# Kernel tuning notes

Hardware: AMD Instinct MI355X
Metric: run time of the kernel (lower is better)

## Reference

```python
import jax, jax.numpy as jnp
import numpy as np

N_QUBITS = 6
BLOCKS = 3
LATENT = 3
DIM = 1 << N_QUBITS  # 64, state-vector size
BATCH = 131072
INP_DIM = 6  # must equal N_QUBITS (repo applies linear_pre to the n_qubits-dim recon)

# Wire 0 is the most-significant qubit (PennyLane convention).
_idx = np.arange(DIM)
BITS = ((_idx[:, None] >> (N_QUBITS - 1 - np.arange(N_QUBITS))) & 1)  # (64, 6)
# Chain of CZ(k, k+1): all diagonal, fold into one sign vector per block.
CZ_SIGN = jnp.asarray(np.prod(1 - 2 * (BITS[:, :-1] * BITS[:, 1:]), axis=1).astype(np.float32))  # (64,)
Z_SIGNS = jnp.asarray((1 - 2 * BITS).astype(np.float32))  # (64, 6): <Z_k> signs per basis state


def _apply_1q(state, U, wire):
    # state: (B, 64) complex64; U: (2,2) complex64 acting on `wire`
    B = state.shape[0]
    s = state.reshape(B, 1 << wire, 2, 1 << (N_QUBITS - 1 - wire))
    s = jnp.einsum('ij,bxjy->bxiy', U, s)
    return s.reshape(B, DIM)


def _circuit(amps, weights, n_out):
    # AmplitudeEmbedding with normalize=True (x was already unit-normed in torch; idempotent)
    norm = jnp.linalg.norm(amps, axis=1, keepdims=True)
    state = (amps / norm).astype(jnp.complex64)  # (B, 64)
    for j in range(BLOCKS):
        for k in range(N_QUBITS):
            tx = weights[j, k, 0]
            tz = weights[j, k, 1]
            c = jnp.cos(0.5 * tx).astype(jnp.complex64)
            s = jnp.sin(0.5 * tx).astype(jnp.complex64)
            em = jnp.exp(-0.5j * tz).astype(jnp.complex64)
            ep = jnp.exp(0.5j * tz).astype(jnp.complex64)
            # Fused U = RZ(tz) @ RX(tx)
            U = jnp.stack([jnp.stack([em * c, -1j * em * s]),
                           jnp.stack([-1j * ep * s, ep * c])])
            state = _apply_1q(state, U, k)
        state = state * CZ_SIGN  # all CZ gates of the block, fused
    probs = state.real ** 2 + state.imag ** 2  # (B, 64)
    return probs @ Z_SIGNS[:, :n_out]  # expval(PauliZ(k)) for k < n_out


def setup_inputs() -> dict:
    key = jax.random.key(0)
    k1, k2, k3, k4, k5 = jax.random.split(key, 5)
    x = jax.random.normal(k1, (BATCH, INP_DIM), dtype=jnp.float32)
    bound = 1.0 / np.sqrt(INP_DIM)
    W_pre = jax.random.uniform(k2, (DIM, INP_DIM), minval=-bound, maxval=bound, dtype=jnp.float32)
    b_pre = jax.random.uniform(k3, (DIM,), minval=-bound, maxval=bound, dtype=jnp.float32)
    enc_w = jax.random.normal(k4, (BLOCKS, N_QUBITS, 3), dtype=jnp.float32) * 0.01
    dec_w = jax.random.normal(k5, (BLOCKS, N_QUBITS, 3), dtype=jnp.float32) * 0.01
    return {'x': x, 'W_pre': W_pre, 'b_pre': b_pre, 'enc_w': enc_w, 'dec_w': dec_w}


def reference(x, W_pre, b_pre, enc_w, dec_w):
    h = jnp.tanh(x @ W_pre.T + b_pre)                     # (B, 64)
    latent = _circuit(h, enc_w, LATENT)                    # (B, 3)
    padded = jnp.zeros((x.shape[0], DIM), jnp.float32).at[:, :LATENT].set(latent)
    recon = _circuit(padded, dec_w, N_QUBITS)              # (B, 6)
    reconstructed = jnp.tanh(recon @ W_pre.T + b_pre)      # (B, 64)
    return reconstructed, latent
```

## Files before the change

kernel.cpp:

```cpp
#include <hip/hip_runtime.h>

#define BATCH 131072

typedef float v2f __attribute__((ext_vector_type(2)));

__device__ __forceinline__ float fast_tanh(float v) {
    float e = __expf(2.0f * v);
    return 1.0f - 2.0f / (e + 1.0f);
}

template <int CTRL>
__device__ __forceinline__ float dppf(float v) {
    return __int_as_float(__builtin_amdgcn_update_dpp(
        0, __float_as_int(v), CTRL, 0xF, 0xF, true));
}
#define DPP_XOR1 0xB1
#define DPP_XOR2 0x4E

__device__ __forceinline__ v2f swap2(v2f v) { return __builtin_shufflevector(v, v, 1, 0); }

template <int MASK>
__device__ __forceinline__ void rx_pairs(v2f* zr, v2f* zi, float c, float s) {
#pragma unroll
    for (int j = 0; j < 8; ++j) {
        if (j & MASK) continue;
        int j1 = j | MASK;
        v2f ar = zr[j], ai = zi[j], br = zr[j1], bi = zi[j1];
        zr[j]  = c * ar + s * bi;
        zi[j]  = c * ai - s * br;
        zr[j1] = c * br + s * ai;
        zi[j1] = c * bi - s * ar;
    }
}

template <int CTRL>
__device__ __forceinline__ void rx_exch2(v2f* zr, v2f* zi, float c, float s) {
#pragma unroll
    for (int j = 0; j < 8; ++j) {
        v2f pr, pi;
        pr.x = dppf<CTRL>(zr[j].x);
        pr.y = dppf<CTRL>(zr[j].y);
        pi.x = dppf<CTRL>(zi[j].x);
        pi.y = dppf<CTRL>(zi[j].y);
        v2f mr = zr[j], mi = zi[j];
        zr[j] = c * mr + s * pi;
        zi[j] = c * mi - s * pr;
    }
}

__device__ __forceinline__ void enc_tail(v2f* zr, v2f* zi, const float* rx,
                                         const float* sDblk, int sub) {
    rx_pairs<2>(zr, zi, rx[2], rx[3]);
    rx_pairs<1>(zr, zi, rx[4], rx[5]);
    {
        float c = rx[6], s = rx[7];
#pragma unroll
        for (int j = 0; j < 8; ++j) {
            v2f orr = zr[j], oi = zi[j];
            zr[j] = c * orr + s * swap2(oi);
            zi[j] = c * oi - s * swap2(orr);
        }
    }
    rx_exch2<DPP_XOR2>(zr, zi, rx[8], rx[9]);
    rx_exch2<DPP_XOR1>(zr, zi, rx[10], rx[11]);
#pragma unroll
    for (int j = 0; j < 8; ++j) {
        float4 d = *(const float4*)&sDblk[(j * 4 + sub) * 4];
        v2f dr = {d.x, d.y}, di = {d.z, d.w};
        v2f orr = zr[j], oi = zi[j];
        zr[j] = dr * orr - di * oi;
        zi[j] = dr * oi + di * orr;
    }
}

__global__ __launch_bounds__(256, 4) void qae_fused(const float* __restrict__ x,
                                                    const float* __restrict__ Wp,
                                                    const float* __restrict__ bp,
                                                    const float* __restrict__ enc_w,
                                                    const float* __restrict__ dec_w,
                                                    float* __restrict__ out) {
    __shared__ __align__(16) float shbuf[1344];
    __shared__ float sA[36];
    __shared__ float sRx[36];

    float* gt = shbuf;
    float* Sr = shbuf + 144;
    float* Si = shbuf + 656;
    float* sW = shbuf;
    float* sB = shbuf + 544;
    float* sD = shbuf + 1088;

    const int t = threadIdx.x;
    const int bl = t >> 2;
    const int sub = t & 3;

    const size_t b = (size_t)blockIdx.x * 64 + bl;
    const float* xp = x + b * 6;
    float2 x01 = *(const float2*)(xp);
    float2 x23 = *(const float2*)(xp + 2);
    float2 x45 = *(const float2*)(xp + 4);

    if (t < 18) {
        float tx = dec_w[t * 3 + 0];
        float tz = dec_w[t * 3 + 1];
        float c = cosf(0.5f * tx), s = sinf(0.5f * tx);
        float ch = cosf(0.5f * tz), sh = sinf(0.5f * tz);
        gt[t * 8 + 0] = c * ch;  gt[t * 8 + 1] = -c * sh;
        gt[t * 8 + 2] = -s * sh; gt[t * 8 + 3] = -s * ch;
        gt[t * 8 + 4] = s * sh;  gt[t * 8 + 5] = -s * ch;
        gt[t * 8 + 6] = c * ch;  gt[t * 8 + 7] = c * sh;
        float etx = enc_w[t * 3 + 0];
        float ec = cosf(0.5f * etx), es = sinf(0.5f * etx);
        if (t >= 12) {
            sRx[2 * t] = ec * ec - es * es;
            sRx[2 * t + 1] = 4.0f * ec * es;
        } else {
            sRx[2 * t] = ec;
            sRx[2 * t + 1] = es;
        }
    }
    const int cl = t & 7;
    const int pr = t >> 3;
    for (int f = t; f < 512; f += 256) {
        int r = f >> 3, c = f & 7;
        Sr[f] = (r == c && c < 3) ? 1.0f : 0.0f;
        Si[f] = 0.0f;
    }

    for (int bb = 0; bb < 3; ++bb) {
        for (int w = 0; w < 6; ++w) {
            __syncthreads();
            int g = bb * 6 + w;
            int p = 5 - w;
            float u00r = gt[g * 8 + 0], u00i = gt[g * 8 + 1], u01r = gt[g * 8 + 2], u01i = gt[g * 8 + 3];
            float u10r = gt[g * 8 + 4], u10i = gt[g * 8 + 5], u11r = gt[g * 8 + 6], u11i = gt[g * 8 + 7];
            int r0 = ((pr >> p) << (p + 1)) | (pr & ((1 << p) - 1));
            int r1 = r0 | (1 << p);
            float ar = Sr[r0 * 8 + cl], ai = Si[r0 * 8 + cl];
            float br = Sr[r1 * 8 + cl], bi = Si[r1 * 8 + cl];
            Sr[r0 * 8 + cl] = u00r * ar - u00i * ai + u01r * br - u01i * bi;
            Si[r0 * 8 + cl] = u00r * ai + u00i * ar + u01r * bi + u01i * br;
            Sr[r1 * 8 + cl] = u10r * ar - u10i * ai + u11r * br - u11i * bi;
            Si[r1 * 8 + cl] = u10r * ai + u10i * ar + u11r * bi + u11i * br;
        }
        __syncthreads();
        for (int f = t; f < 512; f += 256) {
            int r = f >> 3;
            if (__popc(r & (r >> 1)) & 1) {
                Sr[f] = -Sr[f];
                Si[f] = -Si[f];
            }
        }
    }
    __syncthreads();

    if (t < 36) {
        int k = t / 6, i = t % 6;
        int d = (i < 3) ? i : ((i == 5) ? 1 : 0);
        int e = (i < 3) ? i : ((i == 3) ? 1 : 2);
        float acc = 0.0f;
        for (int r = 0; r < 64; ++r) {
            float term = Sr[r * 8 + d] * Sr[r * 8 + e] + Si[r * 8 + d] * Si[r * 8 + e];
            acc += ((r >> (5 - k)) & 1) ? -term : term;
        }
        if (i >= 3) acc *= 2.0f;
        sA[t] = acc;
    }
    __syncthreads();

    for (int f = t; f < 512; f += 256) {
        int g = f >> 4, e = f & 15;
        int j = g >> 2, su = g & 3;
        float val;
        if (e < 12)      { int row = 8 * j + su + 4 * (e & 1); val = Wp[row * 6 + (e >> 1)]; }
        else if (e < 14) { int row = 8 * j + su + 4 * (e - 12); val = bp[row]; }
        else val = 0.0f;
        sW[g * 16 + j * 4 + e] = val;
    }
    if (t < 64) {
        float w0 = Wp[t * 6 + 0], w1 = Wp[t * 6 + 1], w2 = Wp[t * 6 + 2];
        float w3 = Wp[t * 6 + 3], w4 = Wp[t * 6 + 4], w5 = Wp[t * 6 + 5];
        int basep = 8 * t + ((t >> 4) << 2);
#pragma unroll
        for (int i = 0; i < 6; ++i) {
            float acc = w0 * sA[0 * 6 + i] + w1 * sA[1 * 6 + i] + w2 * sA[2 * 6 + i]
                      + w3 * sA[3 * 6 + i] + w4 * sA[4 * 6 + i] + w5 * sA[5 * 6 + i];
            sB[basep + i] = acc;
        }
        sB[basep + 6] = bp[t];
        sB[basep + 7] = 0.0f;
    }
    if (t >= 64 && t < 192) {
        int idx = t - 64;
        int bb = idx >> 6, r = idx & 63;
        float phi = 0.0f;
        for (int k = 0; k < 6; ++k) {
            float tz = enc_w[(bb * 6 + k) * 3 + 1];
            phi += ((r >> (5 - k)) & 1) ? 0.5f * tz : -0.5f * tz;
        }
        float sgn = (__popc(r & (r >> 1)) & 1) ? -1.0f : 1.0f;
        int su = r & 3, m = r >> 2, j = m >> 1, hm = m & 1;
        int base = ((bb * 8 + j) * 4 + su) * 4;
        sD[base + hm]     = sgn * cosf(phi);
        sD[base + 2 + hm] = sgn * sinf(phi);
    }
    __syncthreads();

    float xv[6] = {x01.x, x01.y, x23.x, x23.y, x45.x, x45.y};

    v2f zr[8], zi[8];
    v2f S2 = {0.0f, 0.0f};
#pragma unroll
    for (int j = 0; j < 8; ++j) {
        const float* wb = &sW[(j * 4 + sub) * 16 + j * 4];
        float4 c0 = *(const float4*)wb;
        float4 c1 = *(const float4*)(wb + 4);
        float4 c2 = *(const float4*)(wb + 8);
        float4 c3 = *(const float4*)(wb + 12);
        v2f a = {c3.x, c3.y};
        a += xv[0] * (v2f){c0.x, c0.y};
        a += xv[1] * (v2f){c0.z, c0.w};
        a += xv[2] * (v2f){c1.x, c1.y};
        a += xv[3] * (v2f){c1.z, c1.w};
        a += xv[4] * (v2f){c2.x, c2.y};
        a += xv[5] * (v2f){c2.z, c2.w};
        v2f th = {fast_tanh(a.x), fast_tanh(a.y)};
        zr[j] = th;
        S2 += th * th;
    }
    float S = S2.x + S2.y;
    S += dppf<DPP_XOR1>(S);
    S += dppf<DPP_XOR2>(S);
    float invS = __builtin_amdgcn_rcpf(S);

    {
        const float* rx = sRx;
        float c = rx[0], s = rx[1];
#pragma unroll
        for (int j = 0; j < 4; ++j) {
            v2f a = zr[j], b2 = zr[j + 4];
            zr[j]     = c * a;
            zi[j]     = -s * b2;
            zr[j + 4] = c * b2;
            zi[j + 4] = -s * a;
        }
        enc_tail(zr, zi, rx, sD, sub);
    }
    {
        const float* rx = sRx + 12;
        rx_pairs<4>(zr, zi, rx[0], rx[1]);
        enc_tail(zr, zi, rx, sD + 128, sub);
    }

    v2f L0 = {0, 0}, L1 = {0, 0}, L2 = {0, 0};
#pragma unroll
    for (int j = 0; j < 8; ++j) {
        v2f p = zr[j] * zr[j] + zi[j] * zi[j];
        L0 += (j & 4) ? -p : p;
        L1 += (j & 2) ? -p : p;
        L2 += (j & 1) ? -p : p;
    }
    v2f Y0 = {0, 0}, Y1 = {0, 0}, Y2 = {0, 0};
#pragma unroll
    for (int j = 0; j < 4; ++j)
        Y0 += zr[j] * zi[j | 4] - zi[j] * zr[j | 4];
#pragma unroll
    for (int j0 = 0; j0 < 8; j0 += 4)
#pragma unroll
        for (int j = j0; j < j0 + 2; ++j)
            Y1 += zr[j] * zi[j | 2] - zi[j] * zr[j | 2];
#pragma unroll
    for (int j = 0; j < 8; j += 2)
        Y2 += zr[j] * zi[j | 1] - zi[j] * zr[j | 1];

    const float* p2 = sRx + 24;
    float t0 = p2[0] * (L0.x + L0.y) + p2[1] * (Y0.x + Y0.y);
    float t1 = p2[2] * (L1.x + L1.y) + p2[3] * (Y1.x + Y1.y);
    float t2 = p2[4] * (L2.x + L2.y) + p2[5] * (Y2.x + Y2.y);
    t0 += dppf<DPP_XOR1>(t0); t0 += dppf<DPP_XOR2>(t0);
    t1 += dppf<DPP_XOR1>(t1); t1 += dppf<DPP_XOR2>(t1);
    t2 += dppf<DPP_XOR1>(t2); t2 += dppf<DPP_XOR2>(t2);
    float l0 = t0 * invS, l1 = t1 * invS, l2 = t2 * invS;

    if (sub == 0) {
        size_t lo = (size_t)BATCH * 64 + b * 3;
        out[lo]     = l0;
        out[lo + 1] = l1;
        out[lo + 2] = l2;
    }

    float q0 = l0 * l0, q1 = l1 * l1, q2 = l2 * l2;
    float invr2 = __builtin_amdgcn_rcpf(q0 + q1 + q2);
    float qh0 = q0 * invr2, qh1 = q1 * invr2, qh2 = q2 * invr2;
    float qh3 = (l0 * l1) * invr2, qh4 = (l0 * l2) * invr2, qh5 = (l1 * l2) * invr2;

    const float* bB = &sB[132 * sub];
    const size_t ob = b * 64 + 16 * sub;
#pragma unroll
    for (int ch = 0; ch < 4; ++ch) {
        float v4[4];
#pragma unroll
        for (int r = 0; r < 4; ++r) {
            int qq = ch * 4 + r;
            float4 u0 = *(const float4*)&bB[8 * qq];
            float4 u1 = *(const float4*)&bB[8 * qq + 4];
            float acc = u1.z
                      + qh0 * u0.x + qh1 * u0.y + qh2 * u0.z + qh3 * u0.w
                      + qh4 * u1.x + qh5 * u1.y;
            v4[r] = fast_tanh(acc);
        }
        float4 o = {v4[0], v4[1], v4[2], v4[3]};
        *(float4*)&out[ob + ch * 4] = o;
    }
}

extern "C" void kernel_launch(void* const* d_in, const int* in_sizes, int n_in,
                              void* d_out, int out_size, void* d_ws, size_t ws_size,
                              hipStream_t stream) {
    const float* x   = (const float*)d_in[0];
    const float* Wp  = (const float*)d_in[1];
    const float* bpv = (const float*)d_in[2];
    const float* enc = (const float*)d_in[3];
    const float* dec = (const float*)d_in[4];
    float* out = (float*)d_out;

    qae_fused<<<(BATCH * 4) / 256, 256, 0, stream>>>(x, Wp, bpv, enc, dec, out);
}
```

Before: 102.6 us.

## Process two batch tiles per block and shrink decoder-unitary setup to four columns

Each block now handles two 64-sample tiles in a loop, so the per-block setup is amortized over twice the samples and only half as many blocks launch. That setup covers building the decoder unitary through 18 synchronized gate steps, the observable matrix, and the shared weight tables. The unitary scratch is also narrowed from 8 to 4 columns, so one element per thread suffices and only 128 threads do the gate updates. The cost is half as many blocks, and so less parallelism and latency hiding across the GPU. Each thread also holds x values for both tiles in registers.

```diff
diff --git a/kernel.cpp b/kernel.cpp
--- a/kernel.cpp
+++ b/kernel.cpp
@@ -1,6 +1,7 @@
 #include <hip/hip_runtime.h>
 
 #define BATCH 131072
+#define ITERS 2
 
 typedef float v2f __attribute__((ext_vector_type(2)));
 
@@ -85,7 +86,7 @@
 
     float* gt = shbuf;
     float* Sr = shbuf + 144;
-    float* Si = shbuf + 656;
+    float* Si = shbuf + 400;
     float* sW = shbuf;
     float* sB = shbuf + 544;
     float* sD = shbuf + 1088;
@@ -94,11 +95,15 @@
     const int bl = t >> 2;
     const int sub = t & 3;
 
-    const size_t b = (size_t)blockIdx.x * 64 + bl;
-    const float* xp = x + b * 6;
-    float2 x01 = *(const float2*)(xp);
-    float2 x23 = *(const float2*)(xp + 2);
-    float2 x45 = *(const float2*)(xp + 4);
+    const size_t b0 = (size_t)blockIdx.x * (64 * ITERS) + bl;
+    float2 xg[ITERS][3];
+#pragma unroll
+    for (int it = 0; it < ITERS; ++it) {
+        const float* xp = x + (b0 + (size_t)it * 64) * 6;
+        xg[it][0] = *(const float2*)(xp);
+        xg[it][1] = *(const float2*)(xp + 2);
+        xg[it][2] = *(const float2*)(xp + 4);
+    }
 
     if (t < 18) {
         float tx = dec_w[t * 3 + 0];
@@ -119,36 +124,38 @@
             sRx[2 * t + 1] = es;
         }
     }
-    const int cl = t & 7;
-    const int pr = t >> 3;
-    for (int f = t; f < 512; f += 256) {
-        int r = f >> 3, c = f & 7;
-        Sr[f] = (r == c && c < 3) ? 1.0f : 0.0f;
-        Si[f] = 0.0f;
-    }
-
+    {
+        int r = t >> 2, c = t & 3;
+        Sr[t] = (r == c && c < 3) ? 1.0f : 0.0f;
+        Si[t] = 0.0f;
+    }
+
+    const int cl = t & 3;
+    const int pr = t >> 2;
     for (int bb = 0; bb < 3; ++bb) {
         for (int w = 0; w < 6; ++w) {
             __syncthreads();
-            int g = bb * 6 + w;
-            int p = 5 - w;
-            float u00r = gt[g * 8 + 0], u00i = gt[g * 8 + 1], u01r = gt[g * 8 + 2], u01i = gt[g * 8 + 3];
-            float u10r = gt[g * 8 + 4], u10i = gt[g * 8 + 5], u11r = gt[g * 8 + 6], u11i = gt[g * 8 + 7];
-            int r0 = ((pr >> p) << (p + 1)) | (pr & ((1 << p) - 1));
-            int r1 = r0 | (1 << p);
-            float ar = Sr[r0 * 8 + cl], ai = Si[r0 * 8 + cl];
-            float br = Sr[r1 * 8 + cl], bi = Si[r1 * 8 + cl];
-            Sr[r0 * 8 + cl] = u00r * ar - u00i * ai + u01r * br - u01i * bi;
-            Si[r0 * 8 + cl] = u00r * ai + u00i * ar + u01r * bi + u01i * br;
-            Sr[r1 * 8 + cl] = u10r * ar - u10i * ai + u11r * br - u11i * bi;
-            Si[r1 * 8 + cl] = u10r * ai + u10i * ar + u11r * bi + u11i * br;
+            if (t < 128) {
+                int g = bb * 6 + w;
+                int p = 5 - w;
+                float u00r = gt[g * 8 + 0], u00i = gt[g * 8 + 1], u01r = gt[g * 8 + 2], u01i = gt[g * 8 + 3];
+                float u10r = gt[g * 8 + 4], u10i = gt[g * 8 + 5], u11r = gt[g * 8 + 6], u11i = gt[g * 8 + 7];
+                int r0 = ((pr >> p) << (p + 1)) | (pr & ((1 << p) - 1));
+                int r1 = r0 | (1 << p);
+                float ar = Sr[r0 * 4 + cl], ai = Si[r0 * 4 + cl];
+                float br = Sr[r1 * 4 + cl], bi = Si[r1 * 4 + cl];
+                Sr[r0 * 4 + cl] = u00r * ar - u00i * ai + u01r * br - u01i * bi;
+                Si[r0 * 4 + cl] = u00r * ai + u00i * ar + u01r * bi + u01i * br;
+                Sr[r1 * 4 + cl] = u10r * ar - u10i * ai + u11r * br - u11i * bi;
+                Si[r1 * 4 + cl] = u10r * ai + u10i * ar + u11r * bi + u11i * br;
+            }
         }
         __syncthreads();
-        for (int f = t; f < 512; f += 256) {
-            int r = f >> 3;
+        {
+            int r = t >> 2;
             if (__popc(r & (r >> 1)) & 1) {
-                Sr[f] = -Sr[f];
-                Si[f] = -Si[f];
+                Sr[t] = -Sr[t];
+                Si[t] = -Si[t];
             }
         }
     }
@@ -160,7 +167,7 @@
         int e = (i < 3) ? i : ((i == 3) ? 1 : 2);
         float acc = 0.0f;
         for (int r = 0; r < 64; ++r) {
-            float term = Sr[r * 8 + d] * Sr[r * 8 + e] + Si[r * 8 + d] * Si[r * 8 + e];
+            float term = Sr[r * 4 + d] * Sr[r * 4 + e] + Si[r * 4 + d] * Si[r * 4 + e];
             acc += ((r >> (5 - k)) & 1) ? -term : term;
         }
         if (i >= 3) acc *= 2.0f;
@@ -206,111 +213,116 @@
     }
     __syncthreads();
 
-    float xv[6] = {x01.x, x01.y, x23.x, x23.y, x45.x, x45.y};
-
-    v2f zr[8], zi[8];
-    v2f S2 = {0.0f, 0.0f};
-#pragma unroll
-    for (int j = 0; j < 8; ++j) {
-        const float* wb = &sW[(j * 4 + sub) * 16 + j * 4];
-        float4 c0 = *(const float4*)wb;
-        float4 c1 = *(const float4*)(wb + 4);
-        float4 c2 = *(const float4*)(wb + 8);
-        float4 c3 = *(const float4*)(wb + 12);
-        v2f a = {c3.x, c3.y};
-        a += xv[0] * (v2f){c0.x, c0.y};
-        a += xv[1] * (v2f){c0.z, c0.w};
-        a += xv[2] * (v2f){c1.x, c1.y};
-        a += xv[3] * (v2f){c1.z, c1.w};
-        a += xv[4] * (v2f){c2.x, c2.y};
-        a += xv[5] * (v2f){c2.z, c2.w};
-        v2f th = {fast_tanh(a.x), fast_tanh(a.y)};
-        zr[j] = th;
-        S2 += th * th;
-    }
-    float S = S2.x + S2.y;
-    S += dppf<DPP_XOR1>(S);
-    S += dppf<DPP_XOR2>(S);
-    float invS = __builtin_amdgcn_rcpf(S);
-
-    {
-        const float* rx = sRx;
-        float c = rx[0], s = rx[1];
-#pragma unroll
-        for (int j = 0; j < 4; ++j) {
-            v2f a = zr[j], b2 = zr[j + 4];
-            zr[j]     = c * a;
-            zi[j]     = -s * b2;
-            zr[j + 4] = c * b2;
-            zi[j + 4] = -s * a;
-        }
-        enc_tail(zr, zi, rx, sD, sub);
-    }
-    {
-        const float* rx = sRx + 12;
-        rx_pairs<4>(zr, zi, rx[0], rx[1]);
-        enc_tail(zr, zi, rx, sD + 128, sub);
-    }
-
-    v2f L0 = {0, 0}, L1 = {0, 0}, L2 = {0, 0};
-#pragma unroll
-    for (int j = 0; j < 8; ++j) {
-        v2f p = zr[j] * zr[j] + zi[j] * zi[j];
-        L0 += (j & 4) ? -p : p;
-        L1 += (j & 2) ? -p : p;
-        L2 += (j & 1) ? -p : p;
-    }
-    v2f Y0 = {0, 0}, Y1 = {0, 0}, Y2 = {0, 0};
-#pragma unroll
-    for (int j = 0; j < 4; ++j)
-        Y0 += zr[j] * zi[j | 4] - zi[j] * zr[j | 4];
-#pragma unroll
-    for (int j0 = 0; j0 < 8; j0 += 4)
-#pragma unroll
-        for (int j = j0; j < j0 + 2; ++j)
-            Y1 += zr[j] * zi[j | 2] - zi[j] * zr[j | 2];
-#pragma unroll
-    for (int j = 0; j < 8; j += 2)
-        Y2 += zr[j] * zi[j | 1] - zi[j] * zr[j | 1];
-
-    const float* p2 = sRx + 24;
-    float t0 = p2[0] * (L0.x + L0.y) + p2[1] * (Y0.x + Y0.y);
-    float t1 = p2[2] * (L1.x + L1.y) + p2[3] * (Y1.x + Y1.y);
-    float t2 = p2[4] * (L2.x + L2.y) + p2[5] * (Y2.x + Y2.y);
-    t0 += dppf<DPP_XOR1>(t0); t0 += dppf<DPP_XOR2>(t0);
-    t1 += dppf<DPP_XOR1>(t1); t1 += dppf<DPP_XOR2>(t1);
-    t2 += dppf<DPP_XOR1>(t2); t2 += dppf<DPP_XOR2>(t2);
-    float l0 = t0 * invS, l1 = t1 * invS, l2 = t2 * invS;
-
-    if (sub == 0) {
-        size_t lo = (size_t)BATCH * 64 + b * 3;
-        out[lo]     = l0;
-        out[lo + 1] = l1;
-        out[lo + 2] = l2;
-    }
-
-    float q0 = l0 * l0, q1 = l1 * l1, q2 = l2 * l2;
-    float invr2 = __builtin_amdgcn_rcpf(q0 + q1 + q2);
-    float qh0 = q0 * invr2, qh1 = q1 * invr2, qh2 = q2 * invr2;
-    float qh3 = (l0 * l1) * invr2, qh4 = (l0 * l2) * invr2, qh5 = (l1 * l2) * invr2;
-
-    const float* bB = &sB[132 * sub];
-    const size_t ob = b * 64 + 16 * sub;
-#pragma unroll
-    for (int ch = 0; ch < 4; ++ch) {
-        float v4[4];
-#pragma unroll
-        for (int r = 0; r < 4; ++r) {
-            int qq = ch * 4 + r;
-            float4 u0 = *(const float4*)&bB[8 * qq];
-            float4 u1 = *(const float4*)&bB[8 * qq + 4];
-            float acc = u1.z
-                      + qh0 * u0.x + qh1 * u0.y + qh2 * u0.z + qh3 * u0.w
-                      + qh4 * u1.x + qh5 * u1.y;
-            v4[r] = fast_tanh(acc);
-        }
-        float4 o = {v4[0], v4[1], v4[2], v4[3]};
-        *(float4*)&out[ob + ch * 4] = o;
+#pragma unroll 1
+    for (int it = 0; it < ITERS; ++it) {
+        const size_t b = b0 + (size_t)it * 64;
+        float xv[6] = {xg[it][0].x, xg[it][0].y, xg[it][1].x,
+                       xg[it][1].y, xg[it][2].x, xg[it][2].y};
+
+        v2f zr[8], zi[8];
+        v2f S2 = {0.0f, 0.0f};
+#pragma unroll
+        for (int j = 0; j < 8; ++j) {
+            const float* wb = &sW[(j * 4 + sub) * 16 + j * 4];
+            float4 c0 = *(const float4*)wb;
+            float4 c1 = *(const float4*)(wb + 4);
+            float4 c2 = *(const float4*)(wb + 8);
+            float4 c3 = *(const float4*)(wb + 12);
+            v2f a = {c3.x, c3.y};
+            a += xv[0] * (v2f){c0.x, c0.y};
+            a += xv[1] * (v2f){c0.z, c0.w};
+            a += xv[2] * (v2f){c1.x, c1.y};
+            a += xv[3] * (v2f){c1.z, c1.w};
+            a += xv[4] * (v2f){c2.x, c2.y};
+            a += xv[5] * (v2f){c2.z, c2.w};
+            v2f th = {fast_tanh(a.x), fast_tanh(a.y)};
+            zr[j] = th;
+            S2 += th * th;
+        }
+        float S = S2.x + S2.y;
+        S += dppf<DPP_XOR1>(S);
+        S += dppf<DPP_XOR2>(S);
+        float invS = __builtin_amdgcn_rcpf(S);
+
+        {
+            const float* rx = sRx;
+            float c = rx[0], s = rx[1];
+#pragma unroll
+            for (int j = 0; j < 4; ++j) {
+                v2f a = zr[j], b2 = zr[j + 4];
+                zr[j]     = c * a;
+                zi[j]     = -s * b2;
+                zr[j + 4] = c * b2;
+                zi[j + 4] = -s * a;
+            }
+            enc_tail(zr, zi, rx, sD, sub);
+        }
+        {
+            const float* rx = sRx + 12;
+            rx_pairs<4>(zr, zi, rx[0], rx[1]);
+            enc_tail(zr, zi, rx, sD + 128, sub);
+        }
+
+        v2f L0 = {0, 0}, L1 = {0, 0}, L2 = {0, 0};
+#pragma unroll
+        for (int j = 0; j < 8; ++j) {
+            v2f p = zr[j] * zr[j] + zi[j] * zi[j];
+            L0 += (j & 4) ? -p : p;
+            L1 += (j & 2) ? -p : p;
+            L2 += (j & 1) ? -p : p;
+        }
+        v2f Y0 = {0, 0}, Y1 = {0, 0}, Y2 = {0, 0};
+#pragma unroll
+        for (int j = 0; j < 4; ++j)
+            Y0 += zr[j] * zi[j | 4] - zi[j] * zr[j | 4];
+#pragma unroll
+        for (int j0 = 0; j0 < 8; j0 += 4)
+#pragma unroll
+            for (int j = j0; j < j0 + 2; ++j)
+                Y1 += zr[j] * zi[j | 2] - zi[j] * zr[j | 2];
+#pragma unroll
+        for (int j = 0; j < 8; j += 2)
+            Y2 += zr[j] * zi[j | 1] - zi[j] * zr[j | 1];
+
+        const float* p2 = sRx + 24;
+        float t0 = p2[0] * (L0.x + L0.y) + p2[1] * (Y0.x + Y0.y);
+        float t1 = p2[2] * (L1.x + L1.y) + p2[3] * (Y1.x + Y1.y);
+        float t2 = p2[4] * (L2.x + L2.y) + p2[5] * (Y2.x + Y2.y);
+        t0 += dppf<DPP_XOR1>(t0); t0 += dppf<DPP_XOR2>(t0);
+        t1 += dppf<DPP_XOR1>(t1); t1 += dppf<DPP_XOR2>(t1);
+        t2 += dppf<DPP_XOR1>(t2); t2 += dppf<DPP_XOR2>(t2);
+        float l0 = t0 * invS, l1 = t1 * invS, l2 = t2 * invS;
+
+        if (sub == 0) {
+            size_t lo = (size_t)BATCH * 64 + b * 3;
+            out[lo]     = l0;
+            out[lo + 1] = l1;
+            out[lo + 2] = l2;
+        }
+
+        float q0 = l0 * l0, q1 = l1 * l1, q2 = l2 * l2;
+        float invr2 = __builtin_amdgcn_rcpf(q0 + q1 + q2);
+        float qh0 = q0 * invr2, qh1 = q1 * invr2, qh2 = q2 * invr2;
+        float qh3 = (l0 * l1) * invr2, qh4 = (l0 * l2) * invr2, qh5 = (l1 * l2) * invr2;
+
+        const float* bB = &sB[132 * sub];
+        const size_t ob = b * 64 + 16 * sub;
+#pragma unroll
+        for (int ch = 0; ch < 4; ++ch) {
+            float v4[4];
+#pragma unroll
+            for (int r = 0; r < 4; ++r) {
+                int qq = ch * 4 + r;
+                float4 u0 = *(const float4*)&bB[8 * qq];
+                float4 u1 = *(const float4*)&bB[8 * qq + 4];
+                float acc = u1.z
+                          + qh0 * u0.x + qh1 * u0.y + qh2 * u0.z + qh3 * u0.w
+                          + qh4 * u1.x + qh5 * u1.y;
+                v4[r] = fast_tanh(acc);
+            }
+            float4 o = {v4[0], v4[1], v4[2], v4[3]};
+            *(float4*)&out[ob + ch * 4] = o;
+        }
     }
 }
 
@@ -324,5 +336,5 @@
     const float* dec = (const float*)d_in[4];
     float* out = (float*)d_out;
 
-    qae_fused<<<(BATCH * 4) / 256, 256, 0, stream>>>(x, Wp, bpv, enc, dec, out);
-}
+    qae_fused<<<(BATCH * 4) / 256 / ITERS, 256, 0, stream>>>(x, Wp, bpv, enc, dec, out);
+}
```

New measurement: 292.1 us. 2.85x slower.

## Run decoder-unitary setup in one wavefront and overlap table setup on other waves

Applied to the files above, without the earlier changes.

The per-block simulation of the 18 decoder gates on the 64x3 unitary now runs entirely inside the first wavefront. Columns are trimmed from 8 to 4, which removes the 18+ block-wide barriers that separated gate applications. The other waves build the packed weight table (sW) and the diagonal phase table (sD) at the same time, instead of afterwards. Shared buffers are no longer aliased, which raises LDS use per block. Correctness relies on in-order LDS access within a single wavefront.

```diff
diff --git a/kernel.cpp b/kernel.cpp
--- a/kernel.cpp
+++ b/kernel.cpp
@@ -79,16 +79,14 @@
                                                     const float* __restrict__ enc_w,
                                                     const float* __restrict__ dec_w,
                                                     float* __restrict__ out) {
-    __shared__ __align__(16) float shbuf[1344];
+    __shared__ __align__(16) float gt[144];
+    __shared__ __align__(16) float Sr[256];
+    __shared__ __align__(16) float Si[256];
     __shared__ float sA[36];
     __shared__ float sRx[36];
-
-    float* gt = shbuf;
-    float* Sr = shbuf + 144;
-    float* Si = shbuf + 656;
-    float* sW = shbuf;
-    float* sB = shbuf + 544;
-    float* sD = shbuf + 1088;
+    __shared__ __align__(16) float sW[544];
+    __shared__ __align__(16) float sB[544];
+    __shared__ __align__(16) float sD[256];
 
     const int t = threadIdx.x;
     const int bl = t >> 2;
@@ -100,56 +98,93 @@
     float2 x23 = *(const float2*)(xp + 2);
     float2 x45 = *(const float2*)(xp + 4);
 
-    if (t < 18) {
-        float tx = dec_w[t * 3 + 0];
-        float tz = dec_w[t * 3 + 1];
-        float c = cosf(0.5f * tx), s = sinf(0.5f * tx);
-        float ch = cosf(0.5f * tz), sh = sinf(0.5f * tz);
-        gt[t * 8 + 0] = c * ch;  gt[t * 8 + 1] = -c * sh;
-        gt[t * 8 + 2] = -s * sh; gt[t * 8 + 3] = -s * ch;
-        gt[t * 8 + 4] = s * sh;  gt[t * 8 + 5] = -s * ch;
-        gt[t * 8 + 6] = c * ch;  gt[t * 8 + 7] = c * sh;
-        float etx = enc_w[t * 3 + 0];
-        float ec = cosf(0.5f * etx), es = sinf(0.5f * etx);
-        if (t >= 12) {
-            sRx[2 * t] = ec * ec - es * es;
-            sRx[2 * t + 1] = 4.0f * ec * es;
-        } else {
-            sRx[2 * t] = ec;
-            sRx[2 * t + 1] = es;
-        }
-    }
-    const int cl = t & 7;
-    const int pr = t >> 3;
-    for (int f = t; f < 512; f += 256) {
-        int r = f >> 3, c = f & 7;
-        Sr[f] = (r == c && c < 3) ? 1.0f : 0.0f;
-        Si[f] = 0.0f;
-    }
-
-    for (int bb = 0; bb < 3; ++bb) {
-        for (int w = 0; w < 6; ++w) {
-            __syncthreads();
-            int g = bb * 6 + w;
-            int p = 5 - w;
-            float u00r = gt[g * 8 + 0], u00i = gt[g * 8 + 1], u01r = gt[g * 8 + 2], u01i = gt[g * 8 + 3];
-            float u10r = gt[g * 8 + 4], u10i = gt[g * 8 + 5], u11r = gt[g * 8 + 6], u11i = gt[g * 8 + 7];
-            int r0 = ((pr >> p) << (p + 1)) | (pr & ((1 << p) - 1));
-            int r1 = r0 | (1 << p);
-            float ar = Sr[r0 * 8 + cl], ai = Si[r0 * 8 + cl];
-            float br = Sr[r1 * 8 + cl], bi = Si[r1 * 8 + cl];
-            Sr[r0 * 8 + cl] = u00r * ar - u00i * ai + u01r * br - u01i * bi;
-            Si[r0 * 8 + cl] = u00r * ai + u00i * ar + u01r * bi + u01i * br;
-            Sr[r1 * 8 + cl] = u10r * ar - u10i * ai + u11r * br - u11i * bi;
-            Si[r1 * 8 + cl] = u10r * ai + u10i * ar + u11r * bi + u11i * br;
-        }
-        __syncthreads();
-        for (int f = t; f < 512; f += 256) {
-            int r = f >> 3;
-            if (__popc(r & (r >> 1)) & 1) {
-                Sr[f] = -Sr[f];
-                Si[f] = -Si[f];
+    if (t < 64) {
+        if (t < 18) {
+            float tx = dec_w[t * 3 + 0];
+            float tz = dec_w[t * 3 + 1];
+            float c = cosf(0.5f * tx), s = sinf(0.5f * tx);
+            float ch = cosf(0.5f * tz), sh = sinf(0.5f * tz);
+            gt[t * 8 + 0] = c * ch;  gt[t * 8 + 1] = -c * sh;
+            gt[t * 8 + 2] = -s * sh; gt[t * 8 + 3] = -s * ch;
+            gt[t * 8 + 4] = s * sh;  gt[t * 8 + 5] = -s * ch;
+            gt[t * 8 + 6] = c * ch;  gt[t * 8 + 7] = c * sh;
+            float etx = enc_w[t * 3 + 0];
+            float ec = cosf(0.5f * etx), es = sinf(0.5f * etx);
+            if (t >= 12) {
+                sRx[2 * t] = ec * ec - es * es;
+                sRx[2 * t + 1] = 4.0f * ec * es;
+            } else {
+                sRx[2 * t] = ec;
+                sRx[2 * t + 1] = es;
             }
+        }
+#pragma unroll
+        for (int q = 0; q < 4; ++q) {
+            int f = t + 64 * q;
+            int r = f >> 2, c = f & 3;
+            Sr[f] = (r == c && c < 3) ? 1.0f : 0.0f;
+            Si[f] = 0.0f;
+        }
+        const int cl = t & 3;
+        const int pq = t >> 2;
+        for (int bb = 0; bb < 3; ++bb) {
+            for (int w = 0; w < 6; ++w) {
+                int g = bb * 6 + w;
+                int p = 5 - w;
+                float u00r = gt[g * 8 + 0], u00i = gt[g * 8 + 1];
+                float u01r = gt[g * 8 + 2], u01i = gt[g * 8 + 3];
+                float u10r = gt[g * 8 + 4], u10i = gt[g * 8 + 5];
+                float u11r = gt[g * 8 + 6], u11i = gt[g * 8 + 7];
+#pragma unroll
+                for (int h = 0; h < 2; ++h) {
+                    int pp = pq + 16 * h;
+                    int r0 = ((pp >> p) << (p + 1)) | (pp & ((1 << p) - 1));
+                    int r1 = r0 | (1 << p);
+                    float ar = Sr[r0 * 4 + cl], ai = Si[r0 * 4 + cl];
+                    float br = Sr[r1 * 4 + cl], bi = Si[r1 * 4 + cl];
+                    Sr[r0 * 4 + cl] = u00r * ar - u00i * ai + u01r * br - u01i * bi;
+                    Si[r0 * 4 + cl] = u00r * ai + u00i * ar + u01r * bi + u01i * br;
+                    Sr[r1 * 4 + cl] = u10r * ar - u10i * ai + u11r * br - u11i * bi;
+                    Si[r1 * 4 + cl] = u10r * ai + u10i * ar + u11r * bi + u11i * br;
+                }
+            }
+#pragma unroll
+            for (int q = 0; q < 4; ++q) {
+                int f = t + 64 * q;
+                int r = f >> 2;
+                if (__popc(r & (r >> 1)) & 1) {
+                    Sr[f] = -Sr[f];
+                    Si[f] = -Si[f];
+                }
+            }
+        }
+    } else if (t < 192) {
+#pragma unroll
+        for (int q = 0; q < 4; ++q) {
+            int f = (t - 64) + 128 * q;
+            int g = f >> 4, e = f & 15;
+            int j = g >> 2, su = g & 3;
+            float val;
+            if (e < 12)      { int row = 8 * j + su + 4 * (e & 1); val = Wp[row * 6 + (e >> 1)]; }
+            else if (e < 14) { int row = 8 * j + su + 4 * (e - 12); val = bp[row]; }
+            else val = 0.0f;
+            sW[g * 16 + j * 4 + e] = val;
+        }
+    } else {
+#pragma unroll
+        for (int q = 0; q < 2; ++q) {
+            int idx = (t - 192) + 64 * q;
+            int bb = idx >> 6, r = idx & 63;
+            float phi = 0.0f;
+            for (int k = 0; k < 6; ++k) {
+                float tz = enc_w[(bb * 6 + k) * 3 + 1];
+                phi += ((r >> (5 - k)) & 1) ? 0.5f * tz : -0.5f * tz;
+            }
+            float sgn = (__popc(r & (r >> 1)) & 1) ? -1.0f : 1.0f;
+            int su = r & 3, m = r >> 2, j = m >> 1, hm = m & 1;
+            int base = ((bb * 8 + j) * 4 + su) * 4;
+            sD[base + hm]     = sgn * cosf(phi);
+            sD[base + 2 + hm] = sgn * sinf(phi);
         }
     }
     __syncthreads();
@@ -160,7 +195,7 @@
         int e = (i < 3) ? i : ((i == 3) ? 1 : 2);
         float acc = 0.0f;
         for (int r = 0; r < 64; ++r) {
-            float term = Sr[r * 8 + d] * Sr[r * 8 + e] + Si[r * 8 + d] * Si[r * 8 + e];
+            float term = Sr[r * 4 + d] * Sr[r * 4 + e] + Si[r * 4 + d] * Si[r * 4 + e];
             acc += ((r >> (5 - k)) & 1) ? -term : term;
         }
         if (i >= 3) acc *= 2.0f;
@@ -168,15 +203,6 @@
     }
     __syncthreads();
 
-    for (int f = t; f < 512; f += 256) {
-        int g = f >> 4, e = f & 15;
-        int j = g >> 2, su = g & 3;
-        float val;
-        if (e < 12)      { int row = 8 * j + su + 4 * (e & 1); val = Wp[row * 6 + (e >> 1)]; }
-        else if (e < 14) { int row = 8 * j + su + 4 * (e - 12); val = bp[row]; }
-        else val = 0.0f;
-        sW[g * 16 + j * 4 + e] = val;
-    }
     if (t < 64) {
         float w0 = Wp[t * 6 + 0], w1 = Wp[t * 6 + 1], w2 = Wp[t * 6 + 2];
         float w3 = Wp[t * 6 + 3], w4 = Wp[t * 6 + 4], w5 = Wp[t * 6 + 5];
@@ -189,20 +215,6 @@
         }
         sB[basep + 6] = bp[t];
         sB[basep + 7] = 0.0f;
-    }
-    if (t >= 64 && t < 192) {
-        int idx = t - 64;
-        int bb = idx >> 6, r = idx & 63;
-        float phi = 0.0f;
-        for (int k = 0; k < 6; ++k) {
-            float tz = enc_w[(bb * 6 + k) * 3 + 1];
-            phi += ((r >> (5 - k)) & 1) ? 0.5f * tz : -0.5f * tz;
-        }
-        float sgn = (__popc(r & (r >> 1)) & 1) ? -1.0f : 1.0f;
-        int su = r & 3, m = r >> 2, j = m >> 1, hm = m & 1;
-        int base = ((bb * 8 + j) * 4 + su) * 4;
-        sD[base + hm]     = sgn * cosf(phi);
-        sD[base + 2 + hm] = sgn * sinf(phi);
     }
     __syncthreads();
 
```

Measured after the change: 100.3 us. -2.3%, faster.
